# Optimization experiments

Hardware: AMD Instinct MI355X
Metric: run time of the kernel (lower is better)

The kernel has to match this reference:

```python
import jax, jax.numpy as jnp
import numpy as np

B, S, D, H, F = 16, 1024, 256, 8, 1024
HD = D // H  # head_dim = 32
EPS = 1e-5


def setup_inputs() -> dict:
    key = jax.random.key(0)
    ks = jax.random.split(key, 12)
    sc = 0.02
    return {
        "x":      jax.random.normal(ks[0], (B, S, D), dtype=jnp.float32),
        "gamma1": jnp.ones((S, D), dtype=jnp.float32),
        "beta1":  jnp.zeros((S, D), dtype=jnp.float32),
        "Wqkv":   jax.random.normal(ks[1], (3 * D, D), dtype=jnp.float32) * sc,
        "bqkv":   jnp.zeros((3 * D,), dtype=jnp.float32),
        "Wo":     jax.random.normal(ks[2], (D, D), dtype=jnp.float32) * sc,
        "bo":     jnp.zeros((D,), dtype=jnp.float32),
        "gamma2": jnp.ones((S, D), dtype=jnp.float32),
        "beta2":  jnp.zeros((S, D), dtype=jnp.float32),
        "W1":     jax.random.normal(ks[3], (F, D), dtype=jnp.float32) * sc,
        "b1":     jnp.zeros((F,), dtype=jnp.float32),
        "W2":     jax.random.normal(ks[4], (D, F), dtype=jnp.float32) * sc,
        "b2":     jnp.zeros((D,), dtype=jnp.float32),
    }


def _layernorm_2d(x, gamma, beta):
    # normalizes jointly over the last TWO dims (seq, d_model), biased variance
    mean = jnp.mean(x, axis=(-2, -1), keepdims=True)
    var = jnp.mean((x - mean) ** 2, axis=(-2, -1), keepdims=True)
    y = (x - mean) / jnp.sqrt(var + EPS)
    return gamma * y + beta


def _mha(x, Wqkv, bqkv, Wo, bo):
    b, s, d = x.shape
    qkv = x @ Wqkv.T + bqkv                                  # [B,S,3D]
    qkv = qkv.reshape(b, s, H, 3 * HD).transpose(0, 2, 1, 3)  # [B,H,S,3HD]
    q, k, v = jnp.split(qkv, 3, axis=-1)                      # each [B,H,S,HD]
    scores = jnp.einsum("bhqd,bhkd->bhqk", q, k) / np.sqrt(HD).astype(np.float32)
    attn = jax.nn.softmax(scores, axis=-1)                    # [B,H,S,S]
    values = jnp.einsum("bhqk,bhkd->bhqd", attn, v)           # [B,H,S,HD]
    # NOTE: original torch code reshapes (B,H,S,HD)->(B,S,H*HD) WITHOUT permuting
    # back; we faithfully reproduce that (row-major reshape, same as torch).
    values = values.reshape(b, s, H * HD)
    return values @ Wo.T + bo


def reference(x, gamma1, beta1, Wqkv, bqkv, Wo, bo, gamma2, beta2, W1, b1, W2, b2):
    # pre-norm attention block (dropout is identity at inference)
    h = _layernorm_2d(x, gamma1, beta1)
    h = _mha(h, Wqkv, bqkv, Wo, bo)
    x = x + h
    # pre-norm MLP block
    h = _layernorm_2d(x, gamma2, beta2)
    h = jax.nn.relu(h @ W1.T + b1) @ W2.T + b2
    return x + h
```

## Files before the change

### kernel.cpp

```cpp
#include <hip/hip_runtime.h>
#include <cstdint>
#include <cstddef>

#define SDn (1024*256)

typedef unsigned short u16;
typedef unsigned int   u32;
typedef __bf16 bf16x8 __attribute__((ext_vector_type(8)));
typedef u16    u16x4v __attribute__((ext_vector_type(4)));
typedef u32    u32x4v __attribute__((ext_vector_type(4)));
typedef float  f32x4  __attribute__((ext_vector_type(4)));
typedef float  f32x16 __attribute__((ext_vector_type(16)));

__device__ __forceinline__ u16 f2bf(float f){
  u32 u = __builtin_bit_cast(u32, f);
  u32 r = u + 0x7FFFu + ((u >> 16) & 1u);
  return (u16)(r >> 16);
}
__device__ __forceinline__ float bf2f(u16 v){
  return __builtin_bit_cast(float, (u32)v << 16);
}

#if __has_builtin(__builtin_amdgcn_exp2f)
#define EXP2(x) __builtin_amdgcn_exp2f(x)
#else
#define EXP2(x) exp2f(x)
#endif

__device__ __forceinline__ u32 cvtpk(float a, float b){
  u32 r;
  asm("v_cvt_pk_bf16_f32 %0, %1, %2" : "=v"(r) : "v"(a), "v"(b));
  return r;
}

__device__ __forceinline__ void gll16(const void* g, void* l){
  __builtin_amdgcn_global_load_lds((const __attribute__((address_space(1))) void*)g,
                                   (__attribute__((address_space(3))) void*)l, 16, 0, 0);
}

__global__ void prep(const float* __restrict__ x, float2* __restrict__ part,
                     u16* __restrict__ xb,
                     const float* __restrict__ cw0, const float* __restrict__ cw1,
                     const float* __restrict__ cw2, const float* __restrict__ cw3,
                     u16* __restrict__ co0, u16* __restrict__ co1,
                     u16* __restrict__ co2, u16* __restrict__ co3)
{
  const int bid = blockIdx.x, t = threadIdx.x;
  if (bid < 768){
    int i = bid*256 + t;
    const float* src; u16* dst; int j = i;
    if      (j <  49152){ src = cw0; dst = co0; }
    else if (j <  65536){ src = cw1; dst = co1; j -=  49152; }
    else if (j < 131072){ src = cw2; dst = co2; j -=  65536; }
    else               { src = cw3; dst = co3; j -= 131072; }
    float4 v = ((const float4*)src)[j];
    u16x4v o; o[0]=f2bf(v.x); o[1]=f2bf(v.y); o[2]=f2bf(v.z); o[3]=f2bf(v.w);
    ((u16x4v*)dst)[j] = o;
    return;
  }
  __shared__ float2 red[4];
  const int i = bid - 768;
  const int b = i >> 6, c = i & 63;
  const size_t off = (size_t)b*SDn + (size_t)c*4096;
  const float4* p = (const float4*)(x + off);
  u16x4v* pxb = (u16x4v*)(xb + off);
  float s = 0.f, q = 0.f;
  #pragma unroll
  for (int k=0;k<4;k++){
    float4 v = p[t + k*256];
    s += v.x+v.y+v.z+v.w;
    q += v.x*v.x + v.y*v.y + v.z*v.z + v.w*v.w;
    u16x4v o; o[0]=f2bf(v.x); o[1]=f2bf(v.y); o[2]=f2bf(v.z); o[3]=f2bf(v.w);
    pxb[t + k*256] = o;
  }
  #pragma unroll
  for (int o=32;o;o>>=1){ s += __shfl_down(s,o); q += __shfl_down(q,o); }
  if ((t & 63) == 0) red[t>>6] = make_float2(s,q);
  __syncthreads();
  if (t == 0){
    float S=0.f,Q=0.f;
    #pragma unroll
    for (int k=0;k<4;k++){ S += red[k].x; Q += red[k].y; }
    part[b*64 + c] = make_float2(S,Q);
  }
}

__global__ void ln_apply(const u16* __restrict__ xin, const float* __restrict__ gamma,
                         const float* __restrict__ beta, const float2* __restrict__ part,
                         u16* __restrict__ y)
{
  int b = blockIdx.y, c = blockIdx.x, t = threadIdx.x;
  __shared__ float2 stat;
  if (t < 64){
    float2 v = part[b*64 + t];
    float s = v.x, q = v.y;
    #pragma unroll
    for (int o=32;o;o>>=1){ s += __shfl_down(s,o); q += __shfl_down(q,o); }
    if (t == 0){
      float mean = s / (float)SDn;
      float var  = q / (float)SDn - mean*mean;
      stat = make_float2(mean, rsqrtf(var + 1e-5f));
    }
  }
  __syncthreads();
  const float mean = stat.x, rstd = stat.y;
  const size_t off = (size_t)b*SDn + (size_t)c*4096;
  const u16x4v* px = (const u16x4v*)(xin + off);
  const float4* pg = (const float4*)(gamma + (size_t)c*4096);
  const float4* pb = (const float4*)(beta  + (size_t)c*4096);
  u16x4v* py = (u16x4v*)(y + off);
  #pragma unroll
  for (int i=0;i<4;i++){
    u16x4v xv = px[t + i*256];
    float4 gv = pg[t + i*256];
    float4 bv = pb[t + i*256];
    u16x4v o;
    o[0] = f2bf(gv.x*(bf2f(xv[0])-mean)*rstd + bv.x);
    o[1] = f2bf(gv.y*(bf2f(xv[1])-mean)*rstd + bv.y);
    o[2] = f2bf(gv.z*(bf2f(xv[2])-mean)*rstd + bv.z);
    o[3] = f2bf(gv.w*(bf2f(xv[3])-mean)*rstd + bv.w);
    py[t + i*256] = o;
  }
}

template<int EPI>
__launch_bounds__(256, 4)
__global__ void gemm128(const u16* __restrict__ A, const u16* __restrict__ W,
                        const float* __restrict__ bias,
                        u16* __restrict__ o0, u16* __restrict__ o1, u16* __restrict__ o2,
                        int K, int N)
{
  __shared__ u16 As[2][4096];
  __shared__ u16 Bs[2][4096];
  const int tid  = threadIdx.x;
  const int lane = tid & 63;
  const int wid  = tid >> 6;
  const int wm = wid >> 1, wn = wid & 1;
  const int g  = lane >> 4;
  const int lr = lane & 15;
  const int m0 = blockIdx.x * 128;
  const int n0 = blockIdx.y * 128;

  f32x4 zf = {0.f,0.f,0.f,0.f};
  f32x4 acc[4][4];
  #pragma unroll
  for (int i=0;i<4;i++)
    #pragma unroll
    for (int j=0;j<4;j++) acc[i][j] = zf;

  const int r0 = tid >> 2, c0 = tid & 3;
  const int cs = c0 ^ ((r0 >> 1) & 3);
  const u16* Ar0 = A + (size_t)(m0 + r0     )*K + cs*8;
  const u16* Ar1 = A + (size_t)(m0 + r0 + 64)*K + cs*8;
  const u16* Wr0 = W + (size_t)(n0 + r0     )*K + cs*8;
  const u16* Wr1 = W + (size_t)(n0 + r0 + 64)*K + cs*8;

  int aoff[4], boff[4];
  #pragma unroll
  for (int m=0;m<4;m++){
    int ra = wm*64 + m*16 + lr;
    aoff[m] = (ra*4 + (g ^ ((ra>>1)&3))) * 8;
    int rb = wn*64 + m*16 + lr;
    boff[m] = (rb*4 + (g ^ ((rb>>1)&3))) * 8;
  }

  auto STAGE = [&](int buf, int k0){
    gll16(Ar0 + k0, &As[buf][tid*8]);
    gll16(Ar1 + k0, &As[buf][(tid+256)*8]);
    gll16(Wr0 + k0, &Bs[buf][tid*8]);
    gll16(Wr1 + k0, &Bs[buf][(tid+256)*8]);
  };

  STAGE(0, 0);
  __syncthreads();
  int cur = 0;
  for (int k0 = 0; k0 < K; k0 += 32){
    if (k0 + 32 < K) STAGE(cur^1, k0 + 32);
    bf16x8 af[4], bfv[4];
    #pragma unroll
    for (int m=0;m<4;m++) af[m]  = *(const bf16x8*)(&As[cur][aoff[m]]);
    #pragma unroll
    for (int n=0;n<4;n++) bfv[n] = *(const bf16x8*)(&Bs[cur][boff[n]]);
    #pragma unroll
    for (int m=0;m<4;m++)
      #pragma unroll
      for (int n=0;n<4;n++)
        acc[m][n] = __builtin_amdgcn_mfma_f32_16x16x32_bf16(af[m], bfv[n], acc[m][n], 0, 0, 0);
    __syncthreads();
    cur ^= 1;
  }

  #pragma unroll
  for (int m=0;m<4;m++){
    const int rowb = m0 + wm*64 + m*16 + g*4;
    #pragma unroll
    for (int n=0;n<4;n++){
      const int col = n0 + wn*64 + n*16 + lr;
      const float bc = bias[col];
      if constexpr (EPI == 0){
        const int hh  = col / 96;
        const int rem = col - hh*96;
        const int which = rem >> 5;
        const int d = rem & 31;
        const int b = rowb >> 10, s0 = rowb & 1023;
        if (which == 2){
          u16x4v pv;
          #pragma unroll
          for (int rr=0;rr<4;rr++) pv[rr] = f2bf(acc[m][n][rr] + bc);
          *(u16x4v*)(o2 + ((size_t)((b*8 + hh)*32 + d))*1024 + s0) = pv;
        } else {
          #pragma unroll
          for (int rr=0;rr<4;rr++){
            float v = acc[m][n][rr] + bc;
            if (which == 0)
              o0[((size_t)((b*8 + hh)*1024 + s0 + rr))*32 + d] = f2bf(v * (0.17677669529663689f * 1.4426950408889634f));
            else
              o1[((size_t)((b*8 + hh)*1024 + s0 + rr))*32 + d] = f2bf(v);
          }
        }
      } else {
        #pragma unroll
        for (int rr=0;rr<4;rr++){
          float v = acc[m][n][rr] + bc;
          o0[(size_t)(rowb + rr) * N + col] = f2bf(v > 0.f ? v : 0.f);
        }
      }
    }
  }
}

__launch_bounds__(256, 4)
__global__ void gemm64(const u16* __restrict__ A, const u16* __restrict__ W,
                       const float* __restrict__ bias, const u16* __restrict__ res,
                       float* __restrict__ outF, int K, int N)
{
  __shared__ u16 As[2][2048];
  __shared__ u16 Bs[2][4096];
  const int tid  = threadIdx.x;
  const int lane = tid & 63;
  const int wid  = tid >> 6;
  const int g  = lane >> 4;
  const int lr = lane & 15;
  const int m0 = blockIdx.x * 64;
  const int n0 = blockIdx.y * 128;

  f32x4 zf = {0.f,0.f,0.f,0.f};
  f32x4 acc[4][2];
  #pragma unroll
  for (int i=0;i<4;i++){ acc[i][0]=zf; acc[i][1]=zf; }

  const int r0 = tid >> 2, c0 = tid & 3;
  const int cs = c0 ^ ((r0 >> 1) & 3);
  const u16* Asrc  = A + (size_t)(m0 + r0)*K + cs*8;
  const u16* Wsrc0 = W + (size_t)(n0 + r0     )*K + cs*8;
  const u16* Wsrc1 = W + (size_t)(n0 + r0 + 64)*K + cs*8;

  int aoff[4], boff[2];
  #pragma unroll
  for (int m=0;m<4;m++){
    int ra = m*16 + lr;
    aoff[m] = (ra*4 + (g ^ ((ra>>1)&3))) * 8;
  }
  #pragma unroll
  for (int n=0;n<2;n++){
    int rb = wid*32 + n*16 + lr;
    boff[n] = (rb*4 + (g ^ ((rb>>1)&3))) * 8;
  }

  auto STAGE = [&](int buf, int k0){
    gll16(Asrc  + k0, &As[buf][tid*8]);
    gll16(Wsrc0 + k0, &Bs[buf][tid*8]);
    gll16(Wsrc1 + k0, &Bs[buf][(tid+256)*8]);
  };

  STAGE(0, 0);
  __syncthreads();
  int cur = 0;
  for (int k0 = 0; k0 < K; k0 += 32){
    if (k0 + 32 < K) STAGE(cur^1, k0 + 32);
    bf16x8 af[4], bfv[2];
    #pragma unroll
    for (int m=0;m<4;m++) af[m]  = *(const bf16x8*)(&As[cur][aoff[m]]);
    #pragma unroll
    for (int n=0;n<2;n++) bfv[n] = *(const bf16x8*)(&Bs[cur][boff[n]]);
    #pragma unroll
    for (int m=0;m<4;m++)
      #pragma unroll
      for (int n=0;n<2;n++)
        acc[m][n] = __builtin_amdgcn_mfma_f32_16x16x32_bf16(af[m], bfv[n], acc[m][n], 0, 0, 0);
    __syncthreads();
    cur ^= 1;
  }

  #pragma unroll
  for (int m=0;m<4;m++){
    const int rowb = m0 + m*16 + g*4;
    #pragma unroll
    for (int n=0;n<2;n++){
      const int col = n0 + wid*32 + n*16 + lr;
      const float bc = bias[col];
      #pragma unroll
      for (int rr=0;rr<4;rr++){
        size_t idx = (size_t)(rowb + rr) * N + col;
        outF[idx] = bf2f(res[idx]) + acc[m][n][rr] + bc;
      }
    }
  }
}

__launch_bounds__(256, 4)
__global__ void attn32f(const u16* __restrict__ Q, const u16* __restrict__ Kb,
                        const u16* __restrict__ Vt, const u16* __restrict__ Wob,
                        const float* __restrict__ bo, const u16* __restrict__ xb,
                        u16* __restrict__ x1b, float2* __restrict__ part2)
{
  __shared__ u16 smem[20480];
  const int tid  = threadIdx.x;
  const int lane = tid & 63;
  const int wid  = tid >> 6;
  const int l31  = lane & 31;
  const int l5   = lane >> 5;
  const int lr   = lane & 15;
  const int g    = lane >> 4;
  const int bh = blockIdx.x;
  const int qx = blockIdx.y;
  const int q0 = qx * 128;
  const size_t base = (size_t)bh * (1024*32);

  const int qrow = q0 + wid*32 + l31;
  const bf16x8 qf0 = *(const bf16x8*)(Q + base + (size_t)qrow*32 + l5*8);
  const bf16x8 qf1 = *(const bf16x8*)(Q + base + (size_t)qrow*32 + 16 + l5*8);

  f32x16 acc = {};
  float lsum = 0.f;

  const int kr = tid >> 2, kc = tid & 3;
  const int vd = tid >> 4, vc = tid & 15;
  const u16* Ksrc0 = Kb + base + (size_t)(kr     )*32 + (kc ^ (kr&3))*8;
  const u16* Ksrc1 = Kb + base + (size_t)(kr + 64)*32 + (kc ^ (kr&3))*8;
  const u16* Vsrc0 = Vt + base + (size_t)(vd     )*1024 + (vc ^ (vd&15))*8;
  const u16* Vsrc1 = Vt + base + (size_t)(vd + 16)*1024 + (vc ^ (vd&15))*8;

  auto STAGE = [&](int buf, int kv0){
    u16* KsB = smem + buf*4096;
    u16* VsB = smem + 8192 + buf*4096;
    gll16(Ksrc0 + (size_t)kv0*32, KsB + tid*8);
    gll16(Ksrc1 + (size_t)kv0*32, KsB + (tid+256)*8);
    gll16(Vsrc0 + kv0, VsB + tid*8);
    gll16(Vsrc1 + kv0, VsB + (tid+256)*8);
  };

  STAGE(0, 0);
  __syncthreads();
  int cur = 0;
  for (int kv0 = 0; kv0 < 1024; kv0 += 128){
    if (kv0 + 128 < 1024) STAGE(cur^1, kv0 + 128);
    const u16* KsC = smem + cur*4096;
    const u16* VsC = smem + 8192 + cur*4096;

    #pragma unroll
    for (int G=0; G<4; ++G){
      const u16* ksb = KsC + (32*G + l31)*32;
      const int sw = l31 & 3;
      bf16x8 kf0 = *(const bf16x8*)(ksb + (((0|l5) ^ sw) << 3));
      bf16x8 kf1 = *(const bf16x8*)(ksb + (((2|l5) ^ sw) << 3));
      f32x16 sf = __builtin_amdgcn_mfma_f32_32x32x16_bf16(kf0, qf0, (f32x16){}, 0, 0, 0);
      sf = __builtin_amdgcn_mfma_f32_32x32x16_bf16(kf1, qf1, sf, 0, 0, 0);

      u32 W[8];
      #pragma unroll
      for (int j=0;j<4;j++){
        float p0 = EXP2(sf[4*j+0]);
        float p1 = EXP2(sf[4*j+1]);
        float p2 = EXP2(sf[4*j+2]);
        float p3 = EXP2(sf[4*j+3]);
        lsum += (p0 + p1) + (p2 + p3);
        W[2*j+0] = cvtpk(p0, p1);
        W[2*j+1] = cvtpk(p2, p3);
      }

      #pragma unroll
      for (int sl=0; sl<2; ++sl){
        u32 a0 = W[4*sl + 0], b0 = W[4*sl + 2];
        u32 a1 = W[4*sl + 1], b1 = W[4*sl + 3];
        asm("v_permlane32_swap_b32 %0, %1" : "+v"(a0), "+v"(b0));
        asm("v_permlane32_swap_b32 %0, %1" : "+v"(a1), "+v"(b1));
        bf16x8 pa = __builtin_bit_cast(bf16x8, (u32x4v){a0, a1, b0, b1});
        const int cp = 4*G + 2*sl + l5;
        bf16x8 vb = *(const bf16x8*)(VsC + l31*128 + ((cp ^ (l31 & 15)) << 3));
        acc = __builtin_amdgcn_mfma_f32_32x32x16_bf16(pa, vb, acc, 0, 0, 0);
      }
    }
    __syncthreads();
    cur ^= 1;
  }

  lsum += __shfl_xor(lsum, 32);
  float inv = 1.0f / lsum;
  u16* T = smem + 16384;
  #pragma unroll
  for (int r=0;r<16;r++){
    int qloc = (r&3) + 8*(r>>2) + 4*l5;
    float iv = __shfl(inv, qloc);
    int row = wid*4 + (r>>2);
    int col = ((r&3) + 4*l5)*32 + l31;
    int ch  = col >> 3;
    T[row*256 + ((ch ^ row) << 3) + (col & 7)] = f2bf(acc[r] * iv);
  }

  auto stageWo = [&](int buf, int k0){
    u16* dst = smem + buf*8192;
    #pragma unroll
    for (int j=0;j<4;j++){
      int ch = tid + j*256;
      int n = ch >> 2, c = ch & 3;
      int kcc = c ^ ((n>>1)&3);
      gll16(Wob + (size_t)n*256 + k0 + kcc*8, dst + ch*8);
    }
  };
  stageWo(0, 0);
  __syncthreads();

  f32x4 zf4 = {0.f,0.f,0.f,0.f};
  f32x4 acc2[4] = {zf4, zf4, zf4, zf4};
  int cw = 0;
  #pragma unroll
  for (int kk=0; kk<8; ++kk){
    if (kk < 7) stageWo(cw^1, (kk+1)*32);
    bf16x8 af = *(const bf16x8*)(T + lr*256 + (((4*kk + g) ^ lr) << 3));
    #pragma unroll
    for (int nt=0; nt<4; ++nt){
      int n = wid*64 + nt*16 + lr;
      bf16x8 bw = *(const bf16x8*)(smem + cw*8192 + n*32 + ((g ^ ((n>>1)&3)) << 3));
      acc2[nt] = __builtin_amdgcn_mfma_f32_16x16x32_bf16(af, bw, acc2[nt], 0, 0, 0);
    }
    __syncthreads();
    cw ^= 1;
  }

  const int b = bh >> 3, h = bh & 7;
  const int srow0 = h*128 + qx*16;
  float ss = 0.f, qq = 0.f;
  #pragma unroll
  for (int nt=0; nt<4; ++nt){
    int col = wid*64 + nt*16 + lr;
    float bc = bo[col];
    #pragma unroll
    for (int rr=0; rr<4; ++rr){
      int row = g*4 + rr;
      size_t idx = ((size_t)b*1024 + srow0 + row)*256 + col;
      float v = bf2f(xb[idx]) + acc2[nt][rr] + bc;
      x1b[idx] = f2bf(v);
      ss += v; qq += v*v;
    }
  }
  #pragma unroll
  for (int o=32;o;o>>=1){ ss += __shfl_down(ss,o); qq += __shfl_down(qq,o); }
  float2* sred = (float2*)smem;
  if (lane == 0) sred[wid] = make_float2(ss, qq);
  __syncthreads();
  if (tid == 0){
    float S=0.f, QQ=0.f;
    #pragma unroll
    for (int k2=0;k2<4;k2++){ S += sred[k2].x; QQ += sred[k2].y; }
    part2[b*64 + h*8 + qx] = make_float2(S, QQ);
  }
}

extern "C" void kernel_launch(void* const* d_in, const int* in_sizes, int n_in,
                              void* d_out, int out_size, void* d_ws, size_t ws_size,
                              hipStream_t stream)
{
  const float* x      = (const float*)d_in[0];
  const float* gamma1 = (const float*)d_in[1];
  const float* beta1  = (const float*)d_in[2];
  const float* Wqkv   = (const float*)d_in[3];
  const float* bqkv   = (const float*)d_in[4];
  const float* Wo     = (const float*)d_in[5];
  const float* bo     = (const float*)d_in[6];
  const float* gamma2 = (const float*)d_in[7];
  const float* beta2  = (const float*)d_in[8];
  const float* W1     = (const float*)d_in[9];
  const float* b1     = (const float*)d_in[10];
  const float* W2     = (const float*)d_in[11];
  const float* b2     = (const float*)d_in[12];
  float* out = (float*)d_out;
  char* ws = (char*)d_ws;

  float2* part  = (float2*)(ws + 256);
  float2* part2 = (float2*)(ws + 8448);
  u16* wq   = (u16*)(ws + 16896);
  u16* wo   = (u16*)(ws + 410112);
  u16* w1   = (u16*)(ws + 541184);
  u16* w2   = (u16*)(ws + 1065472);
  u16* hbuf = (u16*)(ws + 1589760);
  u16* qb   = (u16*)(ws + 9978368);
  u16* kb   = (u16*)(ws + 18366976);
  u16* vtb  = (u16*)(ws + 26755584);
  u16* xb   = (u16*)(ws + 35144192);
  u16* midb = (u16*)(ws + 9978368);
  u16* x1b  = (u16*)(ws + 43532800);

  prep<<<1792, 256, 0, stream>>>(x, part, xb, Wqkv, Wo, W1, W2, wq, wo, w1, w2);

  ln_apply<<<dim3(64,16), 256, 0, stream>>>(xb, gamma1, beta1, part, hbuf);

  gemm128<0><<<dim3(128,6), 256, 0, stream>>>(hbuf, wq, bqkv, qb, kb, vtb, 256, 768);

  attn32f<<<dim3(128,8), 256, 0, stream>>>(qb, kb, vtb, wo, bo, xb, x1b, part2);

  ln_apply<<<dim3(64,16), 256, 0, stream>>>(x1b, gamma2, beta2, part2, hbuf);

  gemm128<2><<<dim3(128,8), 256, 0, stream>>>(hbuf, w1, b1, midb, nullptr, nullptr, 256, 1024);

  gemm64<<<dim3(256,2), 256, 0, stream>>>(midb, w2, b2, x1b, out, 1024, 256);
}
```

Baseline: 107.6 us.

## Fuse MLP up and down projections into one kernel keeping hidden tile in LDS

Replaces the separate W1 GEMM (with ReLU) and W2 GEMM with one kernel. Each block takes 32 rows, computes 128-wide hidden chunks with 32x32 MFMAs, writes the ReLU'd bf16 chunk into swizzled LDS, and accumulates into the output right away. This removes the 32 MB hidden activation round-trip through global memory and one launch. The cost is a smaller M tile (32 rows), so weights are reloaded per block, and 512 blocks at two-block occupancy run with heavier LDS use and more syncs per step.

```diff
diff --git a/kernel.cpp b/kernel.cpp
--- a/kernel.cpp
+++ b/kernel.cpp
@@ -123,7 +123,6 @@
   }
 }
 
-template<int EPI>
 __launch_bounds__(256, 4)
 __global__ void gemm128(const u16* __restrict__ A, const u16* __restrict__ W,
                         const float* __restrict__ bias,
@@ -197,112 +196,25 @@
     for (int n=0;n<4;n++){
       const int col = n0 + wn*64 + n*16 + lr;
       const float bc = bias[col];
-      if constexpr (EPI == 0){
-        const int hh  = col / 96;
-        const int rem = col - hh*96;
-        const int which = rem >> 5;
-        const int d = rem & 31;
-        const int b = rowb >> 10, s0 = rowb & 1023;
-        if (which == 2){
-          u16x4v pv;
-          #pragma unroll
-          for (int rr=0;rr<4;rr++) pv[rr] = f2bf(acc[m][n][rr] + bc);
-          *(u16x4v*)(o2 + ((size_t)((b*8 + hh)*32 + d))*1024 + s0) = pv;
-        } else {
-          #pragma unroll
-          for (int rr=0;rr<4;rr++){
-            float v = acc[m][n][rr] + bc;
-            if (which == 0)
-              o0[((size_t)((b*8 + hh)*1024 + s0 + rr))*32 + d] = f2bf(v * (0.17677669529663689f * 1.4426950408889634f));
-            else
-              o1[((size_t)((b*8 + hh)*1024 + s0 + rr))*32 + d] = f2bf(v);
-          }
-        }
+      const int hh  = col / 96;
+      const int rem = col - hh*96;
+      const int which = rem >> 5;
+      const int d = rem & 31;
+      const int b = rowb >> 10, s0 = rowb & 1023;
+      if (which == 2){
+        u16x4v pv;
+        #pragma unroll
+        for (int rr=0;rr<4;rr++) pv[rr] = f2bf(acc[m][n][rr] + bc);
+        *(u16x4v*)(o2 + ((size_t)((b*8 + hh)*32 + d))*1024 + s0) = pv;
       } else {
         #pragma unroll
         for (int rr=0;rr<4;rr++){
           float v = acc[m][n][rr] + bc;
-          o0[(size_t)(rowb + rr) * N + col] = f2bf(v > 0.f ? v : 0.f);
+          if (which == 0)
+            o0[((size_t)((b*8 + hh)*1024 + s0 + rr))*32 + d] = f2bf(v * (0.17677669529663689f * 1.4426950408889634f));
+          else
+            o1[((size_t)((b*8 + hh)*1024 + s0 + rr))*32 + d] = f2bf(v);
         }
-      }
-    }
-  }
-}
-
-__launch_bounds__(256, 4)
-__global__ void gemm64(const u16* __restrict__ A, const u16* __restrict__ W,
-                       const float* __restrict__ bias, const u16* __restrict__ res,
-                       float* __restrict__ outF, int K, int N)
-{
-  __shared__ u16 As[2][2048];
-  __shared__ u16 Bs[2][4096];
-  const int tid  = threadIdx.x;
-  const int lane = tid & 63;
-  const int wid  = tid >> 6;
-  const int g  = lane >> 4;
-  const int lr = lane & 15;
-  const int m0 = blockIdx.x * 64;
-  const int n0 = blockIdx.y * 128;
-
-  f32x4 zf = {0.f,0.f,0.f,0.f};
-  f32x4 acc[4][2];
-  #pragma unroll
-  for (int i=0;i<4;i++){ acc[i][0]=zf; acc[i][1]=zf; }
-
-  const int r0 = tid >> 2, c0 = tid & 3;
-  const int cs = c0 ^ ((r0 >> 1) & 3);
-  const u16* Asrc  = A + (size_t)(m0 + r0)*K + cs*8;
-  const u16* Wsrc0 = W + (size_t)(n0 + r0     )*K + cs*8;
-  const u16* Wsrc1 = W + (size_t)(n0 + r0 + 64)*K + cs*8;
-
-  int aoff[4], boff[2];
-  #pragma unroll
-  for (int m=0;m<4;m++){
-    int ra = m*16 + lr;
-    aoff[m] = (ra*4 + (g ^ ((ra>>1)&3))) * 8;
-  }
-  #pragma unroll
-  for (int n=0;n<2;n++){
-    int rb = wid*32 + n*16 + lr;
-    boff[n] = (rb*4 + (g ^ ((rb>>1)&3))) * 8;
-  }
-
-  auto STAGE = [&](int buf, int k0){
-    gll16(Asrc  + k0, &As[buf][tid*8]);
-    gll16(Wsrc0 + k0, &Bs[buf][tid*8]);
-    gll16(Wsrc1 + k0, &Bs[buf][(tid+256)*8]);
-  };
-
-  STAGE(0, 0);
-  __syncthreads();
-  int cur = 0;
-  for (int k0 = 0; k0 < K; k0 += 32){
-    if (k0 + 32 < K) STAGE(cur^1, k0 + 32);
-    bf16x8 af[4], bfv[2];
-    #pragma unroll
-    for (int m=0;m<4;m++) af[m]  = *(const bf16x8*)(&As[cur][aoff[m]]);
-    #pragma unroll
-    for (int n=0;n<2;n++) bfv[n] = *(const bf16x8*)(&Bs[cur][boff[n]]);
-    #pragma unroll
-    for (int m=0;m<4;m++)
-      #pragma unroll
-      for (int n=0;n<2;n++)
-        acc[m][n] = __builtin_amdgcn_mfma_f32_16x16x32_bf16(af[m], bfv[n], acc[m][n], 0, 0, 0);
-    __syncthreads();
-    cur ^= 1;
-  }
-
-  #pragma unroll
-  for (int m=0;m<4;m++){
-    const int rowb = m0 + m*16 + g*4;
-    #pragma unroll
-    for (int n=0;n<2;n++){
-      const int col = n0 + wid*32 + n*16 + lr;
-      const float bc = bias[col];
-      #pragma unroll
-      for (int rr=0;rr<4;rr++){
-        size_t idx = (size_t)(rowb + rr) * N + col;
-        outF[idx] = bf2f(res[idx]) + acc[m][n][rr] + bc;
       }
     }
   }
@@ -464,6 +376,128 @@
     #pragma unroll
     for (int k2=0;k2<4;k2++){ S += sred[k2].x; QQ += sred[k2].y; }
     part2[b*64 + h*8 + qx] = make_float2(S, QQ);
+  }
+}
+
+__launch_bounds__(256, 2)
+__global__ void mlp_fused(const u16* __restrict__ h, const u16* __restrict__ W1b,
+                          const float* __restrict__ b1, const u16* __restrict__ W2b,
+                          const float* __restrict__ b2, const u16* __restrict__ x1b,
+                          float* __restrict__ out)
+{
+  __shared__ u16 W1s[2][4096];
+  __shared__ u16 mids[4096];
+  __shared__ u16 W2s[2][8192];
+  const int tid = threadIdx.x;
+  const int lane = tid & 63;
+  const int wid = tid >> 6;
+  const int l31 = lane & 31;
+  const int l5  = lane >> 5;
+  const int m0 = blockIdx.x * 32;
+
+  bf16x8 hf[16];
+  {
+    const u16* hrow = h + (size_t)(m0 + l31)*256 + l5*8;
+    #pragma unroll
+    for (int i=0;i<16;i++) hf[i] = *(const bf16x8*)(hrow + i*16);
+  }
+
+  f32x16 oacc0 = {}, oacc1 = {};
+
+  const int w1f  = tid >> 2, w1c = tid & 3;
+  const int w1cs = w1c ^ ((w1f >> 1) & 3);
+  const int w2n  = tid >> 2, w2c = tid & 3;
+  auto stageW1 = [&](int buf, int f0, int k0){
+    gll16(W1b + (size_t)(f0 + w1f)*256 + k0 + w1cs*8, &W1s[buf][tid*8]);
+    int f2 = w1f + 64;
+    int cs2 = w1c ^ ((f2 >> 1) & 3);
+    gll16(W1b + (size_t)(f0 + f2)*256 + k0 + cs2*8, &W1s[buf][(tid+256)*8]);
+  };
+  auto stageW2 = [&](int buf, int f0){
+    #pragma unroll
+    for (int j=0;j<4;j++){
+      int n = w2n + j*64;
+      int cs2 = w2c ^ ((n >> 1) & 3);
+      gll16(W2b + (size_t)n*1024 + f0 + cs2*8, &W2s[buf][(tid + j*256)*8]);
+    }
+  };
+
+  for (int fi = 0; fi < 8; ++fi){
+    const int f0 = fi*128;
+    stageW1(0, f0, 0);
+    __syncthreads();
+    f32x16 macc = {};
+    int c1 = 0;
+    #pragma unroll
+    for (int ks=0; ks<8; ++ks){
+      if (ks < 7) stageW1(c1^1, f0, (ks+1)*32);
+      const int floc = wid*32 + l31;
+      const u16* wrow = &W1s[c1][floc*32];
+      const int sw = (floc >> 1) & 3;
+      bf16x8 a0 = *(const bf16x8*)(wrow + (((0|l5) ^ sw) << 3));
+      bf16x8 a1 = *(const bf16x8*)(wrow + (((2|l5) ^ sw) << 3));
+      macc = __builtin_amdgcn_mfma_f32_32x32x16_bf16(a0, hf[ks*2+0], macc, 0, 0, 0);
+      macc = __builtin_amdgcn_mfma_f32_32x32x16_bf16(a1, hf[ks*2+1], macc, 0, 0, 0);
+      __syncthreads();
+      c1 ^= 1;
+    }
+    #pragma unroll
+    for (int rg=0; rg<4; ++rg){
+      const int fb = wid*32 + 8*rg + 4*l5;
+      float4 bv = *(const float4*)(b1 + f0 + fb);
+      float v0 = fmaxf(macc[4*rg+0] + bv.x, 0.f);
+      float v1 = fmaxf(macc[4*rg+1] + bv.y, 0.f);
+      float v2 = fmaxf(macc[4*rg+2] + bv.z, 0.f);
+      float v3 = fmaxf(macc[4*rg+3] + bv.w, 0.f);
+      uint2 w; w.x = cvtpk(v0, v1); w.y = cvtpk(v2, v3);
+      const int c16 = wid*4 + rg;
+      *(uint2*)(&mids[l31*128 + ((c16 ^ (l31&15)) << 3) + 4*l5]) = w;
+    }
+    stageW2(0, f0);
+    __syncthreads();
+
+    int c2 = 0;
+    #pragma unroll
+    for (int k2=0; k2<4; ++k2){
+      if (k2 < 3) stageW2(c2^1, f0 + (k2+1)*32);
+      bf16x8 ma0, ma1;
+      {
+        int c16a = k2*4 + 0*2 + l5;
+        int c16b = k2*4 + 1*2 + l5;
+        ma0 = *(const bf16x8*)(&mids[l31*128 + ((c16a ^ (l31&15)) << 3)]);
+        ma1 = *(const bf16x8*)(&mids[l31*128 + ((c16b ^ (l31&15)) << 3)]);
+      }
+      #pragma unroll
+      for (int nt=0; nt<2; ++nt){
+        const int n = wid*64 + nt*32 + l31;
+        const u16* w2row = &W2s[c2][n*32];
+        const int sw = (n >> 1) & 3;
+        bf16x8 vb0 = *(const bf16x8*)(w2row + (((0|l5) ^ sw) << 3));
+        bf16x8 vb1 = *(const bf16x8*)(w2row + (((2|l5) ^ sw) << 3));
+        if (nt == 0){
+          oacc0 = __builtin_amdgcn_mfma_f32_32x32x16_bf16(ma0, vb0, oacc0, 0, 0, 0);
+          oacc0 = __builtin_amdgcn_mfma_f32_32x32x16_bf16(ma1, vb1, oacc0, 0, 0, 0);
+        } else {
+          oacc1 = __builtin_amdgcn_mfma_f32_32x32x16_bf16(ma0, vb0, oacc1, 0, 0, 0);
+          oacc1 = __builtin_amdgcn_mfma_f32_32x32x16_bf16(ma1, vb1, oacc1, 0, 0, 0);
+        }
+      }
+      __syncthreads();
+      c2 ^= 1;
+    }
+  }
+
+  #pragma unroll
+  for (int nt=0; nt<2; ++nt){
+    const int n = wid*64 + nt*32 + l31;
+    const float bc = b2[n];
+    #pragma unroll
+    for (int r=0; r<16; ++r){
+      int row = (r&3) + 8*(r>>2) + 4*l5;
+      size_t idx = (size_t)(m0 + row)*256 + n;
+      float v = (nt == 0) ? oacc0[r] : oacc1[r];
+      out[idx] = bf2f(x1b[idx]) + v + bc;
+    }
   }
 }
 
@@ -498,20 +532,17 @@
   u16* kb   = (u16*)(ws + 18366976);
   u16* vtb  = (u16*)(ws + 26755584);
   u16* xb   = (u16*)(ws + 35144192);
-  u16* midb = (u16*)(ws + 9978368);
   u16* x1b  = (u16*)(ws + 43532800);
 
   prep<<<1792, 256, 0, stream>>>(x, part, xb, Wqkv, Wo, W1, W2, wq, wo, w1, w2);
 
   ln_apply<<<dim3(64,16), 256, 0, stream>>>(xb, gamma1, beta1, part, hbuf);
 
-  gemm128<0><<<dim3(128,6), 256, 0, stream>>>(hbuf, wq, bqkv, qb, kb, vtb, 256, 768);
+  gemm128<<<dim3(128,6), 256, 0, stream>>>(hbuf, wq, bqkv, qb, kb, vtb, 256, 768);
 
   attn32f<<<dim3(128,8), 256, 0, stream>>>(qb, kb, vtb, wo, bo, xb, x1b, part2);
 
   ln_apply<<<dim3(64,16), 256, 0, stream>>>(x1b, gamma2, beta2, part2, hbuf);
 
-  gemm128<2><<<dim3(128,8), 256, 0, stream>>>(hbuf, w1, b1, midb, nullptr, nullptr, 256, 1024);
-
-  gemm64<<<dim3(256,2), 256, 0, stream>>>(midb, w2, b2, x1b, out, 1024, 256);
-}
+  mlp_fused<<<512, 256, 0, stream>>>(hbuf, w1, b1, w2, b2, x1b, out);
+}
```

After: 114.9 us. 1.07x slower.
